# Performance work log

Hardware: AMD Instinct MI355X
Metric: run time of the kernel (lower is better)

The kernel has to match this reference:

```python
import jax, jax.numpy as jnp
import numpy as np

B, T, C, H = 8, 1024, 768, 12
HD = C // H  # 64


def setup_inputs() -> dict:
    key = jax.random.key(0)
    ks = jax.random.split(key, 9)
    s = 0.02
    x = jax.random.normal(ks[0], (B, T, C), dtype=jnp.float32)
    mask = jnp.tril(jnp.ones((T, T), dtype=bool))[None, None, :, :]  # causal [1,1,T,T]
    wq = jax.random.normal(ks[1], (C, C), dtype=jnp.float32) * s
    wk = jax.random.normal(ks[2], (C, C), dtype=jnp.float32) * s
    wv = jax.random.normal(ks[3], (C, C), dtype=jnp.float32) * s
    wo = jax.random.normal(ks[4], (C, C), dtype=jnp.float32) * s
    bq = jnp.zeros((C,), dtype=jnp.float32)
    bk = jnp.zeros((C,), dtype=jnp.float32)
    bv = jnp.zeros((C,), dtype=jnp.float32)
    bo = jnp.zeros((C,), dtype=jnp.float32)
    return {"x": x, "mask": mask, "wq": wq, "bq": bq, "wk": wk, "bk": bk,
            "wv": wv, "bv": bv, "wo": wo, "bo": bo}


def reference(x, mask, wq, bq, wk, bk, wv, bv, wo, bo):
    Bx, Tx, Cx = x.shape
    # QKV projections (flax Dense: y = x @ W + b)
    q = (x @ wq + bq).reshape(Bx, Tx, H, HD).transpose(0, 2, 1, 3)  # [B,H,T,hd]
    k = (x @ wk + bk).reshape(Bx, Tx, H, HD).transpose(0, 2, 1, 3)
    v = (x @ wv + bv).reshape(Bx, Tx, H, HD).transpose(0, 2, 1, 3)
    attn = jnp.einsum('bhtd,bhsd->bhts', q, k) / jnp.sqrt(jnp.float32(HD))
    attn = jnp.where(mask, attn, jnp.float32(-1e9))
    attn = jax.nn.softmax(attn, axis=-1)
    out = jnp.einsum('bhts,bhsd->bhtd', attn, v)  # [B,H,T,hd]
    out = out.transpose(0, 2, 1, 3).reshape(Bx, Tx, Cx)
    return out @ wo + bo
```

## Files before the change

kernel.cpp:

```cpp
#include <hip/hip_runtime.h>
#include <hip/hip_bf16.h>

typedef __bf16 bf16_t;
typedef __bf16 bf16x8 __attribute__((ext_vector_type(8)));
typedef float f32x4 __attribute__((ext_vector_type(4)));

#define NB 8
#define NT 1024
#define NC 768
#define NH 12
#define NHD 64

__device__ __forceinline__ f32x4 mfma16(bf16x8 a, bf16x8 b, f32x4 c) {
  return __builtin_amdgcn_mfma_f32_16x16x32_bf16(a, b, c, 0, 0, 0);
}

__device__ __forceinline__ void gld_lds16(const void* g, void* l) {
  __builtin_amdgcn_global_load_lds((const __attribute__((address_space(1))) void*)g,
                                   (__attribute__((address_space(3))) void*)l, 16, 0, 0);
}

__global__ void cvt_x(const float* __restrict__ in, bf16_t* __restrict__ out, int n4) {
  int i = blockIdx.x * blockDim.x + threadIdx.x;
  if (i >= n4) return;
  float4 v = ((const float4*)in)[i];
  bf16_t o[4] = {(bf16_t)v.x, (bf16_t)v.y, (bf16_t)v.z, (bf16_t)v.w};
  *(uint2*)(out + i * 4) = *(uint2*)o;
}

__global__ void transpose_w(const float* __restrict__ wq, const float* __restrict__ wk,
                            const float* __restrict__ wv, const float* __restrict__ wo,
                            bf16_t* __restrict__ wqkvT, bf16_t* __restrict__ woT) {
  __shared__ float tile[32][33];
  const int m = blockIdx.z;
  const float* in = (m == 0) ? wq : (m == 1) ? wk : (m == 2) ? wv : wo;
  bf16_t* out = (m == 3) ? woT : (wqkvT + m * NC * NC);
  const int tx = threadIdx.x & 31, ty = threadIdx.x >> 5;
  const int x = blockIdx.x * 32 + tx;
  const int y0 = blockIdx.y * 32;
#pragma unroll
  for (int i = 0; i < 32; i += 8)
    tile[ty + i][tx] = in[(size_t)(y0 + ty + i) * NC + x];
  __syncthreads();
  const int ox = y0 + tx;
  const int oy0 = blockIdx.x * 32;
#pragma unroll
  for (int i = 0; i < 32; i += 8)
    out[(size_t)(oy0 + ty + i) * NC + ox] = (bf16_t)tile[tx][ty + i];
}

__global__ void transpose_v(const bf16_t* __restrict__ V, bf16_t* __restrict__ VT) {
  __shared__ bf16_t tile[32][33];
  const int bh = blockIdx.z;
  const int x0 = blockIdx.x * 32;
  const int y0 = blockIdx.y * 32;
  const int tx = threadIdx.x & 31, ty = threadIdx.x >> 5;
  const bf16_t* in = V + (size_t)bh * NT * NHD;
  bf16_t* out = VT + (size_t)bh * NHD * NT;
#pragma unroll
  for (int i = 0; i < 32; i += 8)
    tile[ty + i][tx] = in[(size_t)(y0 + ty + i) * NHD + x0 + tx];
  __syncthreads();
#pragma unroll
  for (int i = 0; i < 32; i += 8)
    out[(size_t)(x0 + ty + i) * NT + y0 + tx] = tile[tx][ty + i];
}

template <int MODE, int BM>
__global__ __launch_bounds__(256) void gemm_t(
    const bf16_t* __restrict__ A, const bf16_t* __restrict__ BT, int K,
    const float* __restrict__ b0, const float* __restrict__ b1,
    const float* __restrict__ b2, float* __restrict__ outF,
    bf16_t* __restrict__ out0, bf16_t* __restrict__ out1,
    bf16_t* __restrict__ out2) {
  constexpr int NJ = (BM == 128) ? 4 : 2;
  __shared__ __align__(16) bf16_t lA[BM * 32];
  __shared__ __align__(16) bf16_t lB[128 * 32];
  const int tid = threadIdx.x;
  const int lane = tid & 63, wave = tid >> 6;
  const int quad = lane >> 4, l16 = lane & 15;
  const int bm = blockIdx.x * BM, bn = blockIdx.y * 128;
  const int wm = (BM == 128) ? (wave >> 1) * 64 : 0;
  const int wn = (BM == 128) ? (wave & 1) * 64 : wave * 32;

  const int ra = tid >> 2;
  const int cc = tid & 3;
  const int kca = cc ^ ((ra >> 1) & 3);

  f32x4 acc[NJ][4] = {};
  char* lAb = (char*)lA;
  char* lBb = (char*)lB;

  for (int k0 = 0; k0 < K; k0 += 32) {
    __syncthreads();
    gld_lds16(A + (size_t)(bm + ra) * K + k0 + kca * 8, lAb + wave * 1024);
    if (BM == 128)
      gld_lds16(A + (size_t)(bm + 64 + ra) * K + k0 + kca * 8, lAb + 4096 + wave * 1024);
    gld_lds16(BT + (size_t)(bn + ra) * K + k0 + kca * 8, lBb + wave * 1024);
    gld_lds16(BT + (size_t)(bn + 64 + ra) * K + k0 + kca * 8, lBb + 4096 + wave * 1024);
    __syncthreads();

    bf16x8 af[4], bfr[NJ];
#pragma unroll
    for (int i = 0; i < 4; i++) {
      int row = wm + i * 16 + l16;
      int ch = quad ^ ((row >> 1) & 3);
      af[i] = *(const bf16x8*)(lAb + row * 64 + ch * 16);
    }
#pragma unroll
    for (int j = 0; j < NJ; j++) {
      int row = wn + j * 16 + l16;
      int ch = quad ^ ((row >> 1) & 3);
      bfr[j] = *(const bf16x8*)(lBb + row * 64 + ch * 16);
    }
#pragma unroll
    for (int j = 0; j < NJ; j++)
#pragma unroll
      for (int i = 0; i < 4; i++)
        acc[j][i] = mfma16(bfr[j], af[i], acc[j][i]);
  }

  if (MODE == 0) {
#pragma unroll
    for (int j = 0; j < NJ; j++) {
      int n0 = bn + wn + j * 16 + quad * 4;
      float4 b4 = *(const float4*)(b0 + n0);
      float bb4[4] = {b4.x, b4.y, b4.z, b4.w};
#pragma unroll
      for (int i = 0; i < 4; i++) {
        int m = bm + wm + i * 16 + l16;
        float4 o;
        o.x = acc[j][i][0] + bb4[0];
        o.y = acc[j][i][1] + bb4[1];
        o.z = acc[j][i][2] + bb4[2];
        o.w = acc[j][i][3] + bb4[3];
        *(float4*)(outF + (size_t)m * NC + n0) = o;
      }
    }
  } else {
#pragma unroll
    for (int j = 0; j < NJ; j++) {
      int n0 = bn + wn + j * 16 + quad * 4;
      int sel = n0 / 768;
      int nl = n0 - sel * 768;
      int h = nl >> 6, d0 = nl & 63;
      const float* bp = (sel == 0) ? b0 : (sel == 1) ? b1 : b2;
      bf16_t* dst = (sel == 0) ? out0 : (sel == 1) ? out1 : out2;
      float4 b4 = *(const float4*)(bp + nl);
      float bb4[4] = {b4.x, b4.y, b4.z, b4.w};
      float scl = (sel == 0) ? 0.125f : 1.0f;
#pragma unroll
      for (int i = 0; i < 4; i++) {
        int m = bm + wm + i * 16 + l16;
        int bb = m >> 10, t = m & 1023;
        bf16_t o[4];
#pragma unroll
        for (int r = 0; r < 4; r++)
          o[r] = (bf16_t)((acc[j][i][r] + bb4[r]) * scl);
        *(uint2*)(dst + ((size_t)(bb * NH + h) * NT + t) * NHD + d0) = *(uint2*)o;
      }
    }
  }
}

__global__ __launch_bounds__(256) void attn_fwd(
    const bf16_t* __restrict__ Q, const bf16_t* __restrict__ Kt,
    const bf16_t* __restrict__ VT, bf16_t* __restrict__ AO) {
  __shared__ __align__(16) bf16_t lK[2][64 * 64];
  __shared__ __align__(16) bf16_t lV[2][64 * 64];
  __shared__ __align__(16) bf16_t lP[8][16 * 72];
  const int tid = threadIdx.x, lane = tid & 63, wave = tid >> 6;
  const int quad = lane >> 4, l16 = lane & 15;
  const int bh = blockIdx.x;
  const int bx = blockIdx.y;
  const int b = bh / NH, h = bh - b * NH;
  const int qtA = bx, qtB = 15 - bx;
  const int jmax = qtB;

  const size_t qbase = (size_t)bh * NT;
  const size_t qoffA = (qbase + qtA * 64 + wave * 16 + l16) * NHD;
  const size_t qoffB = (qbase + qtB * 64 + wave * 16 + l16) * NHD;
  const bf16x8 aqA0 = *(const bf16x8*)(Q + qoffA + quad * 8);
  const bf16x8 aqA1 = *(const bf16x8*)(Q + qoffA + 32 + quad * 8);
  const bf16x8 aqB0 = *(const bf16x8*)(Q + qoffB + quad * 8);
  const bf16x8 aqB1 = *(const bf16x8*)(Q + qoffB + 32 + quad * 8);

  f32x4 lsA = {0.f, 0.f, 0.f, 0.f}, lsB = lsA;
  f32x4 OfA[4] = {}, OfB[4] = {};
  const f32x4 zero = {0.f, 0.f, 0.f, 0.f};

  const int sr = tid >> 3;
  const int sc = (tid & 7) ^ (sr & 7);
  const bf16_t* Kg0 = Kt + qbase * NHD;
  const bf16_t* Vg0 = VT + (size_t)bh * 64 * NT;
  const size_t kO0 = (size_t)sr * 64 + sc * 8, kO1 = kO0 + (size_t)32 * 64;
  const size_t vO0 = (size_t)sr * NT + sc * 8, vO1 = vO0 + (size_t)32 * NT;

  bf16_t* lPA = lP[wave * 2 + 0];
  bf16_t* lPB = lP[wave * 2 + 1];
  const int sb = quad ^ (l16 >> 2);

#define STAGE(JT, BUF)                                                  \
  do {                                                                  \
    const bf16_t* Kg_ = Kg0 + (size_t)(JT) * 64 * NHD;                  \
    const bf16_t* Vg_ = Vg0 + (JT) * 64;                                \
    char* dK_ = (char*)lK[BUF] + wave * 1024;                           \
    char* dV_ = (char*)lV[BUF] + wave * 1024;                           \
    gld_lds16(Kg_ + kO0, dK_);                                          \
    gld_lds16(Kg_ + kO1, dK_ + 4096);                                   \
    gld_lds16(Vg_ + vO0, dV_);                                          \
    gld_lds16(Vg_ + vO1, dV_ + 4096);                                   \
  } while (0)

  STAGE(0, 0);

  for (int j = 0; j <= jmax; ++j) {
    const int cur = j & 1;
    __syncthreads();
    if (j < jmax) STAGE(j + 1, cur ^ 1);
    const bf16_t* lKc = lK[cur];
    const bf16_t* lVc = lV[cur];
    const bool actA = (j <= qtA);

    f32x4 sA[4], sB[4];
#pragma unroll
    for (int nn = 0; nn < 4; nn++) {
      int row = nn * 16 + l16;
      int sw = row & 7;
      bf16x8 k0 = *(const bf16x8*)((char*)lKc + row * 128 + (quad ^ sw) * 16);
      bf16x8 k1 = *(const bf16x8*)((char*)lKc + row * 128 + ((quad + 4) ^ sw) * 16);
      sB[nn] = mfma16(aqB0, k0, zero);
      sB[nn] = mfma16(aqB1, k1, sB[nn]);
      if (actA) {
        sA[nn] = mfma16(aqA0, k0, zero);
        sA[nn] = mfma16(aqA1, k1, sA[nn]);
      }
    }

    if (j == qtB) {
#pragma unroll
      for (int nn = 0; nn < 4; nn++) {
        int key = nn * 16 + l16;
#pragma unroll
        for (int r = 0; r < 4; r++) {
          int qrow = wave * 16 + quad * 4 + r;
          if (key > qrow) sB[nn][r] = -1e30f;
        }
      }
    }
    if (actA && j == qtA) {
#pragma unroll
      for (int nn = 0; nn < 4; nn++) {
        int key = nn * 16 + l16;
#pragma unroll
        for (int r = 0; r < 4; r++) {
          int qrow = wave * 16 + quad * 4 + r;
          if (key > qrow) sA[nn][r] = -1e30f;
        }
      }
    }

#pragma unroll
    for (int nn = 0; nn < 4; nn++)
#pragma unroll
      for (int r = 0; r < 4; r++) {
        float pv = __expf(sB[nn][r]);
        lsB[r] += pv;
        lPB[(quad * 4 + r) * 72 + ((nn * 16 + l16) ^ (quad * 8))] = (bf16_t)pv;
      }
    if (actA) {
#pragma unroll
      for (int nn = 0; nn < 4; nn++)
#pragma unroll
        for (int r = 0; r < 4; r++) {
          float pv = __expf(sA[nn][r]);
          lsA[r] += pv;
          lPA[(quad * 4 + r) * 72 + ((nn * 16 + l16) ^ (quad * 8))] = (bf16_t)pv;
        }
    }
    asm volatile("s_waitcnt lgkmcnt(0)" ::: "memory");

    const bf16x8 apB0 = *(const bf16x8*)(lPB + l16 * 72 + sb * 8);
    const bf16x8 apB1 = *(const bf16x8*)(lPB + l16 * 72 + (sb + 4) * 8);
    bf16x8 apA0, apA1;
    if (actA) {
      apA0 = *(const bf16x8*)(lPA + l16 * 72 + sb * 8);
      apA1 = *(const bf16x8*)(lPA + l16 * 72 + (sb + 4) * 8);
    }
#pragma unroll
    for (int dd = 0; dd < 4; dd++) {
      int row = dd * 16 + l16;
      int sw = row & 7;
      bf16x8 v0 = *(const bf16x8*)((char*)lVc + row * 128 + (quad ^ sw) * 16);
      bf16x8 v1 = *(const bf16x8*)((char*)lVc + row * 128 + ((quad + 4) ^ sw) * 16);
      OfB[dd] = mfma16(apB0, v0, OfB[dd]);
      OfB[dd] = mfma16(apB1, v1, OfB[dd]);
      if (actA) {
        OfA[dd] = mfma16(apA0, v0, OfA[dd]);
        OfA[dd] = mfma16(apA1, v1, OfA[dd]);
      }
    }
  }
#undef STAGE

#pragma unroll
  for (int off = 8; off >= 1; off >>= 1)
#pragma unroll
    for (int r = 0; r < 4; r++) {
      lsA[r] += __shfl_xor(lsA[r], off, 64);
      lsB[r] += __shfl_xor(lsB[r], off, 64);
    }

#pragma unroll
  for (int g = 0; g < 2; g++) {
    f32x4* Of = g ? OfB : OfA;
    f32x4& lrun = g ? lsB : lsA;
    const int qt = g ? qtB : qtA;
    f32x4 inv;
#pragma unroll
    for (int r = 0; r < 4; r++) inv[r] = 1.0f / lrun[r];
    const int tq = qt * 64 + wave * 16 + quad * 4;
#pragma unroll
    for (int dd = 0; dd < 4; dd++) {
      int col = h * 64 + dd * 16 + l16;
#pragma unroll
      for (int r = 0; r < 4; r++)
        AO[((size_t)b * NT + tq + r) * NC + col] = (bf16_t)(Of[dd][r] * inv[r]);
    }
  }
}

extern "C" void kernel_launch(void* const* d_in, const int* in_sizes, int n_in,
                              void* d_out, int out_size, void* d_ws, size_t ws_size,
                              hipStream_t stream) {
  const float* x = (const float*)d_in[0];
  const float* wq = (const float*)d_in[2];
  const float* bq = (const float*)d_in[3];
  const float* wk = (const float*)d_in[4];
  const float* bk = (const float*)d_in[5];
  const float* wv = (const float*)d_in[6];
  const float* bv = (const float*)d_in[7];
  const float* wo = (const float*)d_in[8];
  const float* bo = (const float*)d_in[9];

  float* outF = (float*)d_out;
  bf16_t* Qb = (bf16_t*)d_out;
  bf16_t* Vb = Qb + (size_t)NB * NH * NT * NHD;
  bf16_t* ws = (bf16_t*)d_ws;
  bf16_t* xb = ws;
  bf16_t* wqkvT = xb + (size_t)NB * NT * NC;
  bf16_t* woT = wqkvT + (size_t)2304 * 768;
  bf16_t* Kb = woT + (size_t)768 * 768;
  bf16_t* VTb = Kb + (size_t)NB * NH * NT * NHD;
  bf16_t* AO = VTb + (size_t)NB * NH * NT * NHD;

  const int n4 = NB * NT * NC / 4;
  cvt_x<<<(n4 + 255) / 256, 256, 0, stream>>>(x, xb, n4);
  transpose_w<<<dim3(24, 24, 4), 256, 0, stream>>>(wq, wk, wv, wo, wqkvT, woT);
  gemm_t<1, 128><<<dim3(64, 18), 256, 0, stream>>>(xb, wqkvT, NC, bq, bk, bv,
                                                   nullptr, Qb, Kb, Vb);
  transpose_v<<<dim3(2, 32, 96), 256, 0, stream>>>(Vb, VTb);
  attn_fwd<<<dim3(96, 8), 256, 0, stream>>>(Qb, Kb, VTb, AO);
  gemm_t<0, 64><<<dim3(128, 6), 256, 0, stream>>>(AO, woT, NC, bo, nullptr, nullptr,
                                                  outF, nullptr, nullptr, nullptr);
}
```

Measured before the change: 209.5 us.

## Double-buffer GEMM LDS tiles with async prefetch and transpose QKV epilogue

The GEMM kernel now uses two LDS buffers for the A and B tiles. It issues the global_load_lds prefetch for the next K slice right after the barrier and then computes on the current buffer, which hides load latency and drops one barrier per iteration. For the QKV mode it also swaps the MFMA operand order so each lane holds a column. The epilogue then writes scalar bf16 values with one bias load per lane instead of vectorised 8-byte stores. This doubles the LDS footprint, which may cut occupancy, and correctness relies on the barrier waiting for the outstanding async loads.

New measurement: 199.2 us. 4.9% less time.

```diff
diff --git a/kernel.cpp b/kernel.cpp
--- a/kernel.cpp
+++ b/kernel.cpp
@@ -74,8 +74,8 @@
     bf16_t* __restrict__ out0, bf16_t* __restrict__ out1,
     bf16_t* __restrict__ out2) {
   constexpr int NJ = (BM == 128) ? 4 : 2;
-  __shared__ __align__(16) bf16_t lA[BM * 32];
-  __shared__ __align__(16) bf16_t lB[128 * 32];
+  __shared__ __align__(16) bf16_t lA[2][BM * 32];
+  __shared__ __align__(16) bf16_t lB[2][128 * 32];
   const int tid = threadIdx.x;
   const int lane = tid & 63, wave = tid >> 6;
   const int quad = lane >> 4, l16 = lane & 15;
@@ -87,18 +87,31 @@
   const int cc = tid & 3;
   const int kca = cc ^ ((ra >> 1) & 3);
 
-  f32x4 acc[NJ][4] = {};
-  char* lAb = (char*)lA;
-  char* lBb = (char*)lB;
-
-  for (int k0 = 0; k0 < K; k0 += 32) {
+  f32x4 acc[4][4] = {};
+
+  const bf16_t* Ar = A + (size_t)(bm + ra) * K + kca * 8;
+  const bf16_t* Ar2 = A + (size_t)(bm + 64 + ra) * K + kca * 8;
+  const bf16_t* Br = BT + (size_t)(bn + ra) * K + kca * 8;
+  const bf16_t* Br2 = BT + (size_t)(bn + 64 + ra) * K + kca * 8;
+
+#define GSTAGE(K0, BUF)                                       \
+  do {                                                        \
+    char* lAb_ = (char*)lA[BUF] + wave * 1024;                \
+    char* lBb_ = (char*)lB[BUF] + wave * 1024;                \
+    gld_lds16(Ar + (K0), lAb_);                               \
+    if (BM == 128) gld_lds16(Ar2 + (K0), lAb_ + 4096);        \
+    gld_lds16(Br + (K0), lBb_);                               \
+    gld_lds16(Br2 + (K0), lBb_ + 4096);                       \
+  } while (0)
+
+  GSTAGE(0, 0);
+
+  for (int k0 = 0, it = 0; k0 < K; k0 += 32, ++it) {
+    const int cur = it & 1;
     __syncthreads();
-    gld_lds16(A + (size_t)(bm + ra) * K + k0 + kca * 8, lAb + wave * 1024);
-    if (BM == 128)
-      gld_lds16(A + (size_t)(bm + 64 + ra) * K + k0 + kca * 8, lAb + 4096 + wave * 1024);
-    gld_lds16(BT + (size_t)(bn + ra) * K + k0 + kca * 8, lBb + wave * 1024);
-    gld_lds16(BT + (size_t)(bn + 64 + ra) * K + k0 + kca * 8, lBb + 4096 + wave * 1024);
-    __syncthreads();
+    if (k0 + 32 < K) GSTAGE(k0 + 32, cur ^ 1);
+    const char* lAb = (const char*)lA[cur];
+    const char* lBb = (const char*)lB[cur];
 
     bf16x8 af[4], bfr[NJ];
 #pragma unroll
@@ -113,12 +126,21 @@
       int ch = quad ^ ((row >> 1) & 3);
       bfr[j] = *(const bf16x8*)(lBb + row * 64 + ch * 16);
     }
-#pragma unroll
-    for (int j = 0; j < NJ; j++)
+    if (MODE == 0) {
+#pragma unroll
+      for (int j = 0; j < NJ; j++)
+#pragma unroll
+        for (int i = 0; i < 4; i++)
+          acc[j][i] = mfma16(bfr[j], af[i], acc[j][i]);
+    } else {
 #pragma unroll
       for (int i = 0; i < 4; i++)
-        acc[j][i] = mfma16(bfr[j], af[i], acc[j][i]);
+#pragma unroll
+        for (int j = 0; j < NJ; j++)
+          acc[i][j] = mfma16(af[i], bfr[j], acc[i][j]);
+    }
   }
+#undef GSTAGE
 
   if (MODE == 0) {
 #pragma unroll
@@ -140,24 +162,24 @@
   } else {
 #pragma unroll
     for (int j = 0; j < NJ; j++) {
-      int n0 = bn + wn + j * 16 + quad * 4;
-      int sel = n0 / 768;
-      int nl = n0 - sel * 768;
-      int h = nl >> 6, d0 = nl & 63;
+      int n = bn + wn + j * 16 + l16;
+      int sel = n / 768;
+      int nl = n - sel * 768;
+      int h = nl >> 6, d = nl & 63;
       const float* bp = (sel == 0) ? b0 : (sel == 1) ? b1 : b2;
       bf16_t* dst = (sel == 0) ? out0 : (sel == 1) ? out1 : out2;
-      float4 b4 = *(const float4*)(bp + nl);
-      float bb4[4] = {b4.x, b4.y, b4.z, b4.w};
+      float bias = bp[nl];
       float scl = (sel == 0) ? 0.125f : 1.0f;
 #pragma unroll
       for (int i = 0; i < 4; i++) {
-        int m = bm + wm + i * 16 + l16;
-        int bb = m >> 10, t = m & 1023;
-        bf16_t o[4];
-#pragma unroll
-        for (int r = 0; r < 4; r++)
-          o[r] = (bf16_t)((acc[j][i][r] + bb4[r]) * scl);
-        *(uint2*)(dst + ((size_t)(bb * NH + h) * NT + t) * NHD + d0) = *(uint2*)o;
+        int m0 = bm + wm + i * 16 + quad * 4;
+#pragma unroll
+        for (int r = 0; r < 4; r++) {
+          int m = m0 + r;
+          int bb = m >> 10, t = m & 1023;
+          dst[((size_t)(bb * NH + h) * NT + t) * NHD + d] =
+              (bf16_t)((acc[i][j][r] + bias) * scl);
+        }
       }
     }
   }
```
